# Kernel tuning notes

Hardware: AMD Instinct MI355X
Metric: run time of the kernel (lower is better)

Reference implementation:

```python
import jax, jax.numpy as jnp
import numpy as np

B, T, D, H, L, V = 2, 2048, 1024, 16, 12, 50257
HD = D // H          # head size 64
F = 4 * D            # FFN hidden 4096
EPS = 1e-5


def setup_inputs() -> dict:
    key = jax.random.key(0)
    keys = iter(jax.random.split(key, 16))
    n = lambda shape: jax.random.normal(next(keys), shape, jnp.float32) * 0.02
    inp = {
        "x": jax.random.randint(next(keys), (B, T), 0, V),
        "tok_emb": n((V, D)),
        "pos_emb": n((T, D)),
        "ln1_g": jnp.ones((L, D), jnp.float32), "ln1_b": jnp.zeros((L, D), jnp.float32),
        "wq": n((L, D, D)), "bq": jnp.zeros((L, D), jnp.float32),
        "wk": n((L, D, D)), "bk": jnp.zeros((L, D), jnp.float32),
        "wv": n((L, D, D)), "bv": jnp.zeros((L, D), jnp.float32),
        "wo": n((L, D, D)), "bo": jnp.zeros((L, D), jnp.float32),
        "ln2_g": jnp.ones((L, D), jnp.float32), "ln2_b": jnp.zeros((L, D), jnp.float32),
        "w1": n((L, D, F)), "b1": jnp.zeros((L, F), jnp.float32),
        "w2": n((L, F, D)), "b2": jnp.zeros((L, D), jnp.float32),
        "lnf_g": jnp.ones((D,), jnp.float32), "lnf_b": jnp.zeros((D,), jnp.float32),
        "fc_w": n((D, V)), "fc_b": jnp.zeros((V,), jnp.float32),
    }
    return inp


def _layernorm(x, g, b):
    m = jnp.mean(x, axis=-1, keepdims=True)
    v = jnp.var(x, axis=-1, keepdims=True)
    return (x - m) * jax.lax.rsqrt(v + EPS) * g + b


def _forward(x, tok_emb, pos_emb, ln1_g, ln1_b, wq, bq, wk, bk, wv, bv,
             wo, bo, ln2_g, ln2_b, w1, b1, w2, b2, lnf_g, lnf_b, fc_w, fc_b):
    # token + positional embedding (dropout is eval-mode identity)
    h = tok_emb[x] + pos_emb[None]                      # [B,T,D]
    mask = jnp.tril(jnp.ones((T, T), bool))             # causal mask
    scale = HD ** (-0.5)
    for l in range(L):
        # NOTE: original Block applies residual around the POST-norm activation
        hn = _layernorm(h, ln1_g[l], ln1_b[l])
        q = (hn @ wq[l] + bq[l]).reshape(B, T, H, HD)
        k = (hn @ wk[l] + bk[l]).reshape(B, T, H, HD)
        v = (hn @ wv[l] + bv[l]).reshape(B, T, H, HD)
        scores = jnp.einsum('bthd,bshd->bhts', q, k) * scale
        scores = jnp.where(mask[None, None], scores, -jnp.inf)
        attn = jax.nn.softmax(scores, axis=-1)
        o = jnp.einsum('bhts,bshd->bthd', attn, v).reshape(B, T, D)
        h = hn + (o @ wo[l] + bo[l])
        hn2 = _layernorm(h, ln2_g[l], ln2_b[l])
        h = hn2 + (jax.nn.relu(hn2 @ w1[l] + b1[l]) @ w2[l] + b2[l])
    h = _layernorm(h, lnf_g, lnf_b)
    logits = h @ fc_w + fc_b                            # [B,T,V]
    return logits


def reference(x, tok_emb, pos_emb, ln1_g, ln1_b, wq, bq, wk, bk, wv, bv,
              wo, bo, ln2_g, ln2_b, w1, b1, w2, b2, lnf_g, lnf_b, fc_w, fc_b):
    return _forward(x, tok_emb, pos_emb, ln1_g, ln1_b, wq, bq, wk, bk, wv, bv,
                    wo, bo, ln2_g, ln2_b, w1, b1, w2, b2, lnf_g, lnf_b, fc_w, fc_b)
```

## Files before the change

### kernel.cpp

```cpp
#include <hip/hip_runtime.h>

#define BB 2
#define TT 2048
#define DD 1024
#define HH 16
#define LL 12
#define VV 50257
#define VP 50432
#define HDD 64
#define FF 4096
#define MM (BB*TT)
#define QS 3072

typedef __bf16 bf16;
typedef __bf16 bf16x8 __attribute__((ext_vector_type(8)));
typedef __bf16 bf16x4 __attribute__((ext_vector_type(4)));
typedef __bf16 bf16x2 __attribute__((ext_vector_type(2)));
typedef float  f32x4  __attribute__((ext_vector_type(4)));
typedef float  f32x4u __attribute__((ext_vector_type(4), aligned(4)));
typedef unsigned int u32x4 __attribute__((ext_vector_type(4)));

typedef const __attribute__((address_space(1))) void* gas_t;
typedef __attribute__((address_space(3))) void* las_t;

__global__ __launch_bounds__(256) void k_embed(const int* __restrict__ x,
    const float* __restrict__ tok, const float* __restrict__ pos,
    float* __restrict__ h)
{
    int row = blockIdx.x;
    int t   = row & (TT - 1);
    int idx = x[row];
    int c   = threadIdx.x * 4;
    float4 a = *(const float4*)(tok + (size_t)idx * DD + c);
    float4 p = *(const float4*)(pos + (size_t)t   * DD + c);
    a.x += p.x; a.y += p.y; a.z += p.z; a.w += p.w;
    *(float4*)(h + (size_t)row * DD + c) = a;
}

__global__ __launch_bounds__(256) void k_ln(const float* __restrict__ in,
    const float* __restrict__ g, const float* __restrict__ b,
    float* __restrict__ outf, bf16* __restrict__ outb)
{
    int row = blockIdx.x, tid = threadIdx.x;
    const float4 v = *(const float4*)(in + (size_t)row * DD + tid * 4);
    float s  = v.x + v.y + v.z + v.w;
    float s2 = v.x*v.x + v.y*v.y + v.z*v.z + v.w*v.w;
    #pragma unroll
    for (int d = 1; d < 64; d <<= 1) { s += __shfl_xor(s, d); s2 += __shfl_xor(s2, d); }
    __shared__ float red[8];
    __shared__ float mv[2];
    int wid = tid >> 6, lane = tid & 63;
    if (lane == 0) { red[2*wid] = s; red[2*wid+1] = s2; }
    __syncthreads();
    if (tid == 0) {
        float ts  = red[0] + red[2] + red[4] + red[6];
        float ts2 = red[1] + red[3] + red[5] + red[7];
        float mean = ts * (1.0f / DD);
        float var  = ts2 * (1.0f / DD) - mean * mean;
        mv[0] = mean; mv[1] = 1.0f / sqrtf(var + 1e-5f);
    }
    __syncthreads();
    float mean = mv[0], inv = mv[1];
    float4 gg = *(const float4*)(g + tid * 4);
    float4 bb = *(const float4*)(b + tid * 4);
    float o0 = (v.x - mean) * inv * gg.x + bb.x;
    float o1 = (v.y - mean) * inv * gg.y + bb.y;
    float o2 = (v.z - mean) * inv * gg.z + bb.z;
    float o3 = (v.w - mean) * inv * gg.w + bb.w;
    size_t o = (size_t)row * DD + tid * 4;
    if (outf) { float4 r = {o0, o1, o2, o3}; *(float4*)(outf + o) = r; }
    if (outb) {
        bf16x4 r4 = {(bf16)o0, (bf16)o1, (bf16)o2, (bf16)o3};
        *(bf16x4*)(outb + o) = r4;
    }
}

__global__ __launch_bounds__(256) void k_wtrans(
    const float* __restrict__ src, bf16* __restrict__ dst,
    int K, int N, int Npad, size_t srcLS, size_t dstLS)
{
    src += (size_t)blockIdx.z * srcLS;
    dst += (size_t)blockIdx.z * dstLS;
    int k0 = blockIdx.y * 32, n0 = blockIdx.x * 256;
    __shared__ float tile[32][256];
    int tid = threadIdx.x;
    #pragma unroll
    for (int p = 0; p < 8; p++) {
        int kk = p * 4 + (tid >> 6);
        int nn = (tid & 63) * 4;
        const float* sp = src + (size_t)(k0 + kk) * N + n0 + nn;
        f32x4u v = {0.f, 0.f, 0.f, 0.f};
        if (n0 + nn + 3 < N) {
            v = *(const f32x4u*)sp;
        } else {
            #pragma unroll
            for (int i = 0; i < 4; i++)
                if (n0 + nn + i < N) v[i] = sp[i];
        }
        *(f32x4*)&tile[kk][nn] = v;
    }
    __syncthreads();
    int n = n0 + tid;
    if (n < Npad) {
        bf16 rowv[32];
        #pragma unroll
        for (int kk = 0; kk < 32; kk++) rowv[kk] = (bf16)tile[kk][tid];
        bf16* dp = dst + (size_t)n * K + k0;
        #pragma unroll
        for (int s = 0; s < 4; s++)
            *(bf16x8*)(dp + s * 8) = *(const bf16x8*)&rowv[s * 8];
    }
}

__global__ __launch_bounds__(256) void k_biasmerge(
    const float* __restrict__ bq, const float* __restrict__ bk,
    const float* __restrict__ bv, float* __restrict__ dst)
{
    int i = blockIdx.x * 256 + threadIdx.x;
    if (i >= LL * QS) return;
    int l = i / QS, j = i % QS;
    float v = (j < 1024) ? bq[l*1024 + j]
            : (j < 2048) ? bk[l*1024 + j - 1024]
                         : bv[l*1024 + j - 2048];
    dst[i] = v;
}

#define GEMM_EPILOGUE(MI_CNT, WM_STRIDE)                                        \
    bool nalign = ((Nout & 3) == 0);                                            \
    _Pragma("unroll")                                                           \
    for (int mi = 0; mi < MI_CNT; mi++) {                                       \
        int row = m0 + wm*WM_STRIDE + mi*16 + r16;                              \
        _Pragma("unroll")                                                       \
        for (int ni = 0; ni < 4; ni++) {                                        \
            int col0 = n0 + wn*64 + ni*16 + g4*4;                               \
            f32x4 v = acc[mi][ni];                                              \
            float sc = (qpre && col0 < 1024) ? 0.125f : 1.0f;                   \
            if (col0 + 3 < Nout) {                                              \
                if (bias) {                                                     \
                    float4 bi = *(const float4*)(bias + col0);                  \
                    v[0] += bi.x; v[1] += bi.y; v[2] += bi.z; v[3] += bi.w;     \
                }                                                               \
                if (res) {                                                      \
                    float4 rr = *(const float4*)(res + (size_t)row*Nout + col0);\
                    v[0] += rr.x; v[1] += rr.y; v[2] += rr.z; v[3] += rr.w;     \
                }                                                               \
                if (relu) { _Pragma("unroll")                                   \
                    for (int j = 0; j < 4; j++) v[j] = fmaxf(v[j], 0.0f); }     \
                if (outf) {                                                     \
                    float* p = outf + (size_t)row * Nout + col0;                \
                    if (nalign) *(f32x4*)p = v; else *(f32x4u*)p = v;           \
                }                                                               \
                if (outb) {                                                     \
                    bf16x4 o4 = {(bf16)(v[0]*sc), (bf16)(v[1]*sc),              \
                                 (bf16)(v[2]*sc), (bf16)(v[3]*sc)};             \
                    *(bf16x4*)(outb + (size_t)row * Nout + col0) = o4;          \
                }                                                               \
            } else {                                                            \
                _Pragma("unroll")                                               \
                for (int j = 0; j < 4; j++) {                                   \
                    int col = col0 + j;                                         \
                    if (col >= Nout) continue;                                  \
                    float vv = v[j] + (bias ? bias[col] : 0.0f);                \
                    if (res)  vv += res[(size_t)row * Nout + col];              \
                    if (relu) vv = fmaxf(vv, 0.0f);                             \
                    if (outf) outf[(size_t)row * Nout + col] = vv;              \
                    if (outb) outb[(size_t)row * Nout + col] = (bf16)(vv*sc);   \
                }                                                               \
            }                                                                   \
        }                                                                       \
    }

#define BARS { __builtin_amdgcn_sched_barrier(0); __builtin_amdgcn_s_barrier(); }

#define STG2(nn, kk)                                                            \
    do { const int k0_ = (nn)*64 + (kk)*32; const int db_ = (nn)&1;             \
        _Pragma("unroll") for (int i_ = 0; i_ < 2; i_++) {                      \
            int a_ = i_*2048 + tid*8;                                           \
            int sr_ = a_>>6, x_ = (a_&63) ^ ((sr_&7)<<3);                       \
            int r_ = 2*sr_ + (x_>>5), e_ = x_&31;                               \
            __builtin_amdgcn_global_load_lds(                                   \
                (gas_t)(A + (size_t)(m0+r_)*K + k0_+e_),                        \
                (las_t)&lA[db_][kk][a_], 16, 0, 0);                             \
        }                                                                       \
        _Pragma("unroll") for (int i_ = 0; i_ < 2; i_++) {                      \
            int a_ = i_*2048 + tid*8;                                           \
            int sr_ = a_>>6, x_ = (a_&63) ^ ((sr_&7)<<3);                       \
            int r_ = 2*sr_ + (x_>>5), e_ = x_&31;                               \
            __builtin_amdgcn_global_load_lds(                                   \
                (gas_t)(BT + (size_t)(n0+r_)*K + k0_+e_),                       \
                (las_t)&lB[db_][kk][a_], 16, 0, 0);                             \
        }                                                                       \
    } while (0)

#define PH2(nn, kk, sn, sk, wv)                                                 \
    { const int db_ = (nn)&1;                                                   \
        bf16x8 af[4], bfr[4];                                                   \
        _Pragma("unroll") for (int mi = 0; mi < 4; mi++) {                      \
            int row_ = wm*64 + mi*16 + r16;                                     \
            int sr_ = row_>>1;                                                  \
            int xp_ = (((row_&1)<<5) | kfrag) ^ ((sr_&7)<<3);                   \
            af[mi] = *(const bf16x8*)&lA[db_][kk][sr_*64 + xp_];                \
        }                                                                       \
        _Pragma("unroll") for (int ni = 0; ni < 4; ni++) {                      \
            int row_ = wn*64 + ni*16 + r16;                                     \
            int sr_ = row_>>1;                                                  \
            int xp_ = (((row_&1)<<5) | kfrag) ^ ((sr_&7)<<3);                   \
            bfr[ni] = *(const bf16x8*)&lB[db_][kk][sr_*64 + xp_];               \
        }                                                                       \
        bool st_ = (sn) < nt;                                                   \
        if (st_) STG2(sn, sk);                                                  \
        BARS;                                                                   \
        __builtin_amdgcn_s_setprio(1);                                          \
        _Pragma("unroll") for (int mi = 0; mi < 4; mi++)                        \
            _Pragma("unroll") for (int ni = 0; ni < 4; ni++)                    \
                acc[mi][ni] = __builtin_amdgcn_mfma_f32_16x16x32_bf16(          \
                    bfr[ni], af[mi], acc[mi][ni], 0, 0, 0);                     \
        __builtin_amdgcn_s_setprio(0);                                          \
        if (wv) { if (st_) asm volatile("s_waitcnt vmcnt(4)" ::: "memory");     \
                  else     asm volatile("s_waitcnt vmcnt(0)" ::: "memory"); }   \
        BARS;                                                                   \
    }

__global__ __launch_bounds__(256) void k_gemm2(
    const bf16* __restrict__ A, const bf16* __restrict__ BT,
    const float* __restrict__ bias, const float* __restrict__ res,
    float* __restrict__ outf, bf16* __restrict__ outb,
    int K, int Nout, int relu, int mswap, int qpre)
{
    __shared__ alignas(16) bf16 lA[2][2][128 * 32];
    __shared__ alignas(16) bf16 lB[2][2][128 * 32];
    int tid = threadIdx.x;
    int lane = tid & 63, w = tid >> 6;
    int wm = w >> 1, wn = w & 1;
    int nb = mswap ? blockIdx.y : blockIdx.x;
    int mb = mswap ? blockIdx.x : blockIdx.y;
    int n0 = nb * 128, m0 = mb * 128;
    int r16 = lane & 15, g4 = lane >> 4;
    int kfrag = g4 * 8;

    f32x4 acc[4][4];
    const f32x4 fzero = {0.f, 0.f, 0.f, 0.f};
    #pragma unroll
    for (int i = 0; i < 4; i++)
        #pragma unroll
        for (int j = 0; j < 4; j++) acc[i][j] = fzero;

    int nt = K >> 6;
    STG2(0, 0); STG2(0, 1); STG2(1, 0);
    asm volatile("s_waitcnt vmcnt(4)" ::: "memory");
    BARS;
    for (int it2 = 0; it2 < nt; it2 += 2) {
        PH2(it2,     0, it2 + 1, 1, 0);
        PH2(it2,     1, it2 + 2, 0, 1);
        PH2(it2 + 1, 0, it2 + 2, 1, 0);
        PH2(it2 + 1, 1, it2 + 3, 0, 1);
    }
    GEMM_EPILOGUE(4, 64)
}

#define SA3(tile, u)                                                            \
    do { int s_ = tid*8; int rl_ = s_>>6;                                       \
        int x_ = (s_&63) ^ ((rl_&7)<<3);                                        \
        __builtin_amdgcn_global_load_lds(                                       \
            (gas_t)(A + (size_t)(m0 + (u)*64 + rl_)*K + (size_t)(tile)*64 + x_),\
            (las_t)&lA3[(tile)&1][(u)*4096 + s_], 16, 0, 0);                    \
    } while (0)
#define SB3(tile, v)                                                            \
    do { int s_ = tid*8; int rl_ = s_>>6; int lr_ = (v)*64 + rl_;               \
        int r_ = (lr_ < 128) ? ((lr_&31) + ((lr_>>5)<<6))                       \
                             : (32 + ((lr_-128)&31) + (((lr_-128)>>5)<<6));     \
        int x_ = (s_&63) ^ ((rl_&7)<<3);                                        \
        __builtin_amdgcn_global_load_lds(                                       \
            (gas_t)(BT + (size_t)(n0 + r_)*K + (size_t)(tile)*64 + x_),         \
            (las_t)&lB3[(tile)&1][(v)*4096 + s_], 16, 0, 0);                    \
    } while (0)
#define RDA3(dst, mig, mi, kh) { int lr_ = wm*128 + ((mig)*4+(mi))*16 + r16;    \
    dst = *(const bf16x8*)&lA3[db_][lr_*64 + ((((kh)*32) | kfrag) ^ ((lr_&7)<<3))]; }
#define RDB3(dst, ni, kh) { int lr_ = wn*32 + (((ni)&1)<<4) + r16 + (((ni)>=2)?128:0); \
    dst = *(const bf16x8*)&lB3[db_][lr_*64 + ((((kh)*32) | kfrag) ^ ((lr_&7)<<3))]; }
#define MF3(mb_, nb_)                                                           \
    _Pragma("unroll") for (int kh = 0; kh < 2; kh++)                            \
        _Pragma("unroll") for (int mi = 0; mi < 4; mi++)                        \
            _Pragma("unroll") for (int ni = 0; ni < 2; ni++)                    \
                acc[(mb_)+mi][(nb_)+ni] = __builtin_amdgcn_mfma_f32_16x16x32_bf16( \
                    bfr[(nb_)+ni][kh], afr[mi][kh], acc[(mb_)+mi][(nb_)+ni], 0, 0, 0);

#define QUAD3(nn, cs, sn)                                                       \
    { const int db_ = (nn)&1;                                                   \
                                                                        \
      _Pragma("unroll") for (int mi=0;mi<4;mi++){RDA3(afr[mi][0],0,mi,0);RDA3(afr[mi][1],0,mi,1);} \
      _Pragma("unroll") for (int ni=0;ni<2;ni++){RDB3(bfr[ni][0],ni,0);RDB3(bfr[ni][1],ni,1);}     \
      BARS;                                                                     \
      __builtin_amdgcn_s_setprio(1); MF3(0,0); __builtin_amdgcn_s_setprio(0);   \
      BARS;                                                                     \
                                                                        \
      _Pragma("unroll") for (int ni=2;ni<4;ni++){RDB3(bfr[ni][0],ni,0);RDB3(bfr[ni][1],ni,1);}     \
      if (cs) { SA3(sn,0); SA3(sn,2); }                                         \
      BARS;                                                                     \
      __builtin_amdgcn_s_setprio(1); MF3(0,2); __builtin_amdgcn_s_setprio(0);   \
      BARS;                                                                     \
                                                                        \
      _Pragma("unroll") for (int mi=0;mi<4;mi++){RDA3(afr[mi][0],1,mi,0);RDA3(afr[mi][1],1,mi,1);} \
      if (cs) { SB3(sn,0); SB3(sn,1); SB3(sn,2); SB3(sn,3); }                   \
      BARS;                                                                     \
      __builtin_amdgcn_s_setprio(1); MF3(4,0); __builtin_amdgcn_s_setprio(0);   \
      BARS;                                                                     \
                                                                        \
      if (cs) { SA3(sn,1); SA3(sn,3); }                                         \
      BARS;                                                                     \
      __builtin_amdgcn_s_setprio(1); MF3(4,2); __builtin_amdgcn_s_setprio(0);   \
      if (cs) asm volatile("s_waitcnt vmcnt(8)" ::: "memory");                  \
      else    asm volatile("s_waitcnt vmcnt(0)" ::: "memory");                  \
      BARS; }

__global__ __launch_bounds__(512, 2) void k_gemm3(
    const bf16* __restrict__ A, const bf16* __restrict__ BT,
    const float* __restrict__ bias, const float* __restrict__ res,
    float* __restrict__ outf, bf16* __restrict__ outb,
    int K, int Nout, int relu, int mswap, int qpre)
{
    __shared__ alignas(16) bf16 lA3[2][256 * 64];
    __shared__ alignas(16) bf16 lB3[2][256 * 64];
    int tid = threadIdx.x;
    int lane = tid & 63, w = tid >> 6;
    int wm = w >> 2, wn = w & 3;
    int nb = mswap ? blockIdx.y : blockIdx.x;
    int mb = mswap ? blockIdx.x : blockIdx.y;
    int n0 = nb * 256, m0 = mb * 256;
    int r16 = lane & 15, g4 = lane >> 4;
    int kfrag = g4 * 8;

    f32x4 acc[8][4];
    const f32x4 fzero = {0.f, 0.f, 0.f, 0.f};
    #pragma unroll
    for (int i = 0; i < 8; i++)
        #pragma unroll
        for (int j = 0; j < 4; j++) acc[i][j] = fzero;

    bf16x8 afr[4][2];
    bf16x8 bfr[4][2];

    int nt = K >> 6;
    SA3(0,0); SA3(0,1); SA3(0,2); SA3(0,3);
    SB3(0,0); SB3(0,1); SB3(0,2); SB3(0,3);
    SA3(1,0); SA3(1,1); SA3(1,2); SA3(1,3);
    SB3(1,0); SB3(1,1); SB3(1,2); SB3(1,3);
    asm volatile("s_waitcnt vmcnt(8)" ::: "memory");
    BARS;
    for (int it2 = 0; it2 < nt; it2 += 2) {
        bool c2 = (it2 + 2 < nt), c3 = (it2 + 3 < nt);
        QUAD3(it2,     c2, it2 + 2);
        QUAD3(it2 + 1, c3, it2 + 3);
    }
    GEMM_EPILOGUE(8, 128)
}

__global__ __launch_bounds__(256) void k_gemm_f32b(
    const bf16* __restrict__ A, const float* __restrict__ Bm,
    const float* __restrict__ bias, float* __restrict__ outf,
    int M, int N, int K)
{
    __shared__ alignas(16) bf16 lA[128][40];
    __shared__ alignas(16) bf16 lB[128][40];
    int tid  = threadIdx.x;
    int lane = tid & 63, wid = tid >> 6;
    int wm = wid >> 1, wn = wid & 1;
    int m0 = blockIdx.x * 128, n0 = blockIdx.y * 128;
    int r16 = lane & 15, g4 = lane >> 4;

    f32x4 acc[4][4];
    const f32x4 fzero = {0.f, 0.f, 0.f, 0.f};
    #pragma unroll
    for (int i = 0; i < 4; i++)
        #pragma unroll
        for (int j = 0; j < 4; j++) acc[i][j] = fzero;

    int arow = tid >> 2, aseg = tid & 3;
    int bkr  = tid >> 3, bnb  = tid & 7;
    bool nfull = (n0 + 128 <= N);

    for (int k0 = 0; k0 < K; k0 += 32) {
        *(uint4*)&lA[arow][aseg*8] =
            *(const uint4*)(A + (size_t)(m0 + arow) * K + k0 + aseg*8);
        *(uint4*)&lA[arow + 64][aseg*8] =
            *(const uint4*)(A + (size_t)(m0 + arow + 64) * K + k0 + aseg*8);
        const float* bsrc = Bm + (size_t)(k0 + bkr) * N + n0;
        #pragma unroll
        for (int q = 0; q < 4; q++) {
            int n = q*32 + bnb*4;
            #pragma unroll
            for (int i = 0; i < 4; i++) {
                float fv = 0.0f;
                if (nfull || (n0 + n + i < N)) fv = bsrc[n + i];
                lB[n+i][bkr] = (bf16)fv;
            }
        }
        __syncthreads();
        int kb = g4 * 8;
        bf16x8 af[4], bfr[4];
        #pragma unroll
        for (int mi = 0; mi < 4; mi++)
            af[mi] = *(const bf16x8*)&lA[wm*64 + mi*16 + r16][kb];
        #pragma unroll
        for (int ni = 0; ni < 4; ni++)
            bfr[ni] = *(const bf16x8*)&lB[wn*64 + ni*16 + r16][kb];
        #pragma unroll
        for (int mi = 0; mi < 4; mi++)
            #pragma unroll
            for (int ni = 0; ni < 4; ni++)
                acc[mi][ni] = __builtin_amdgcn_mfma_f32_16x16x32_bf16(
                    af[mi], bfr[ni], acc[mi][ni], 0, 0, 0);
        __syncthreads();
    }

    #pragma unroll
    for (int ni = 0; ni < 4; ni++) {
        int col = n0 + wn*64 + ni*16 + r16;
        if (col >= N) continue;
        float bi = bias[col];
        #pragma unroll
        for (int mi = 0; mi < 4; mi++) {
            #pragma unroll
            for (int j = 0; j < 4; j++) {
                int row = m0 + wm*64 + mi*16 + g4*4 + j;
                outf[(size_t)row * N + col] = acc[mi][ni][j] + bi;
            }
        }
    }
}

__global__ __launch_bounds__(512) void k_attn3(
    const bf16* __restrict__ qkv, bf16* __restrict__ o)
{
    __shared__ alignas(16) bf16 lK[64][72];
    __shared__ alignas(16) bf16 lVT[64][72];
    int tid = threadIdx.x, lane = tid & 63, w = tid >> 6;
    int r16 = lane & 15, g4 = lane >> 4;
    int t0 = blockIdx.x * 128;
    int bh = blockIdx.y, bb = bh >> 4, hh = bh & 15;
    const bf16* base = qkv + (size_t)bb * TT * QS + hh * HDD;
    const bf16* kp = base + 1024;
    const bf16* vp = base + 2048;
    bf16* op = o + (size_t)bb * TT * DD + hh * HDD;
    int qrow = t0 + w * 16;

    bf16x8 qf0, qf1;
    {
        const bf16* qr = base + (size_t)(qrow + r16) * QS + g4 * 8;
        qf0 = *(const bf16x8*)qr;
        qf1 = *(const bf16x8*)(qr + 32);
    }

    int krow = tid >> 3, kseg = tid & 7;
    int vsp  = tid >> 4, vseg = tid & 15;

    f32x4 oacc[4];
    const f32x4 fzero = {0.f, 0.f, 0.f, 0.f};
    #pragma unroll
    for (int i = 0; i < 4; i++) oacc[i] = fzero;
    float mrun = -1e30f, lrun = 0.f;

    int send = t0 + 128;
    bf16x8 kr;
    bf16x4 va4, vb4;
    {
        kr  = *(const bf16x8*)(kp + (size_t)krow * QS + kseg * 8);
        va4 = *(const bf16x4*)(vp + (size_t)(2*vsp) * QS + vseg * 4);
        vb4 = *(const bf16x4*)(vp + (size_t)(2*vsp) * QS + QS + vseg * 4);
    }

    for (int s0 = 0; s0 < send; s0 += 64) {
        __syncthreads();
        *(bf16x8*)&lK[krow][kseg*8] = kr;
        #pragma unroll
        for (int i = 0; i < 4; i++) {
            int d = vseg*4 + i;
            int mpr = (vsp >> 2) ^ (d >> 3);
            bf16x2 pv2 = {va4[i], vb4[i]};
            *(unsigned int*)&lVT[d][mpr*8 + (vsp&3)*2] =
                __builtin_bit_cast(unsigned int, pv2);
        }
        if (s0 + 64 < send) {
            kr  = *(const bf16x8*)(kp + (size_t)(s0 + 64 + krow) * QS + kseg * 8);
            va4 = *(const bf16x4*)(vp + (size_t)(s0 + 64 + 2*vsp) * QS + vseg * 4);
            vb4 = *(const bf16x4*)(vp + (size_t)(s0 + 64 + 2*vsp) * QS + QS + vseg * 4);
        }
        __syncthreads();

        if (s0 <= qrow + 15) {
            f32x4 sf[4];
            __builtin_amdgcn_s_setprio(1);
            #pragma unroll
            for (int nf = 0; nf < 4; nf++) {
                sf[nf] = fzero;
                bf16x8 kf0 = *(const bf16x8*)&lK[nf*16 + r16][g4*8];
                bf16x8 kf1 = *(const bf16x8*)&lK[nf*16 + r16][32 + g4*8];
                sf[nf] = __builtin_amdgcn_mfma_f32_16x16x32_bf16(kf0, qf0, sf[nf], 0, 0, 0);
                sf[nf] = __builtin_amdgcn_mfma_f32_16x16x32_bf16(kf1, qf1, sf[nf], 0, 0, 0);
            }
            __builtin_amdgcn_s_setprio(0);
            int qa = qrow + r16;
            if (s0 + 63 > qrow) {
                #pragma unroll
                for (int nf = 0; nf < 4; nf++)
                    #pragma unroll
                    for (int j = 0; j < 4; j++)
                        if (s0 + nf*16 + g4*4 + j > qa) sf[nf][j] = -1e30f;
            }
            float pm = sf[0][0];
            #pragma unroll
            for (int nf = 0; nf < 4; nf++)
                #pragma unroll
                for (int j = 0; j < 4; j++) pm = fmaxf(pm, sf[nf][j]);
            pm = fmaxf(pm, __shfl_xor(pm, 16));
            pm = fmaxf(pm, __shfl_xor(pm, 32));
            bool defer = (__all(pm - mrun <= 8.0f) != 0);
            float al = 1.0f;
            if (!defer) {
                float mn = fmaxf(mrun, pm);
                al = __expf(mrun - mn);
                mrun = mn;
            }
            float ps = 0.f;
            #pragma unroll
            for (int nf = 0; nf < 4; nf++)
                #pragma unroll
                for (int j = 0; j < 4; j++) {
                    float p = __expf(sf[nf][j] - mrun);
                    sf[nf][j] = p;
                    ps += p;
                }
            ps += __shfl_xor(ps, 16);
            ps += __shfl_xor(ps, 32);
            lrun = lrun * al + ps;
            if (!defer) {
                #pragma unroll
                for (int nf = 0; nf < 4; nf++)
                    #pragma unroll
                    for (int j = 0; j < 4; j++) oacc[nf][j] *= al;
            }
            unsigned int pk[4][2];
            #pragma unroll
            for (int nf = 0; nf < 4; nf++) {
                bf16x2 a = {(bf16)sf[nf][0], (bf16)sf[nf][1]};
                bf16x2 b = {(bf16)sf[nf][2], (bf16)sf[nf][3]};
                pk[nf][0] = __builtin_bit_cast(unsigned int, a);
                pk[nf][1] = __builtin_bit_cast(unsigned int, b);
            }
            int srcA = r16 + (2*(g4 & 1))*16;
            int srcB = srcA + 16;
            bool hi2 = (g4 >= 2);
            __builtin_amdgcn_s_setprio(1);
            #pragma unroll
            for (int c = 0; c < 2; c++) {
                unsigned int a0 = __shfl(pk[2*c  ][0], srcA);
                unsigned int a1 = __shfl(pk[2*c+1][0], srcA);
                unsigned int b0 = __shfl(pk[2*c  ][1], srcA);
                unsigned int b1 = __shfl(pk[2*c+1][1], srcA);
                unsigned int e0 = __shfl(pk[2*c  ][0], srcB);
                unsigned int e1 = __shfl(pk[2*c+1][0], srcB);
                unsigned int f0 = __shfl(pk[2*c  ][1], srcB);
                unsigned int f1 = __shfl(pk[2*c+1][1], srcB);
                u32x4 uu = { hi2 ? a1 : a0, hi2 ? b1 : b0,
                             hi2 ? e1 : e0, hi2 ? f1 : f0 };
                bf16x8 pf = __builtin_bit_cast(bf16x8, uu);
                #pragma unroll
                for (int nf = 0; nf < 4; nf++) {
                    int d = nf*16 + r16;
                    int mread = (4*c + g4) ^ (d >> 3);
                    bf16x8 vt = *(const bf16x8*)&lVT[d][mread*8];
                    oacc[nf] = __builtin_amdgcn_mfma_f32_16x16x32_bf16(
                        vt, pf, oacc[nf], 0, 0, 0);
                }
            }
            __builtin_amdgcn_s_setprio(0);
        }
    }

    float inv = 1.0f / lrun;
    #pragma unroll
    for (int nf = 0; nf < 4; nf++) {
        f32x4 ov = oacc[nf];
        bf16x4 o4 = {(bf16)(ov[0]*inv), (bf16)(ov[1]*inv),
                     (bf16)(ov[2]*inv), (bf16)(ov[3]*inv)};
        *(bf16x4*)(op + (size_t)(qrow + r16) * DD + nf*16 + g4*4) = o4;
    }
}

extern "C" void kernel_launch(void* const* d_in, const int* in_sizes, int n_in,
                              void* d_out, int out_size, void* d_ws, size_t ws_size,
                              hipStream_t stream)
{
    (void)in_sizes; (void)n_in; (void)out_size;
    const int*   x    = (const int*)  d_in[0];
    const float* tok  = (const float*)d_in[1];
    const float* pos  = (const float*)d_in[2];
    const float* ln1g = (const float*)d_in[3];
    const float* ln1b = (const float*)d_in[4];
    const float* wq   = (const float*)d_in[5];
    const float* bq   = (const float*)d_in[6];
    const float* wk   = (const float*)d_in[7];
    const float* bk   = (const float*)d_in[8];
    const float* wv   = (const float*)d_in[9];
    const float* bv   = (const float*)d_in[10];
    const float* wo   = (const float*)d_in[11];
    const float* bo   = (const float*)d_in[12];
    const float* ln2g = (const float*)d_in[13];
    const float* ln2b = (const float*)d_in[14];
    const float* w1   = (const float*)d_in[15];
    const float* b1   = (const float*)d_in[16];
    const float* w2   = (const float*)d_in[17];
    const float* b2   = (const float*)d_in[18];
    const float* lnfg = (const float*)d_in[19];
    const float* lnfb = (const float*)d_in[20];
    const float* fcw  = (const float*)d_in[21];
    const float* fcb  = (const float*)d_in[22];

    const size_t MB = (size_t)1 << 20;
    char*  sb   = (char*)d_out;
    float* h    = (float*)(sb);
    float* hn   = (float*)(sb + 16*MB);
    bf16*  hnb  = (bf16*) (sb + 32*MB);
    bf16*  qkv  = (bf16*) (sb + 40*MB);
    bf16*  obuf = (bf16*) (sb + 64*MB);
    bf16*  f1b  = (bf16*) (sb + 72*MB);
    bf16*  WT   = (bf16*) (sb + 104*MB);
    float* bqkv = (float*)(sb + 392*MB);
    bf16*  hfb  = (bf16*) d_ws;

    const size_t LWT = 12582912;
    const size_t FCWT_BYTES = (size_t)VP * DD * 2;
    bool fast_logits = (ws_size >= 8*MB + FCWT_BYTES);
    bf16* fcwT = (bf16*)((char*)d_ws + 8*MB);

    dim3 blk(256);
    dim3 blk512(512);

    k_wtrans<<<dim3(4, 32, 12), blk, 0, stream>>>(wq, WT,               DD, DD, DD, (size_t)DD*DD, LWT);
    k_wtrans<<<dim3(4, 32, 12), blk, 0, stream>>>(wk, WT + 1024*1024,   DD, DD, DD, (size_t)DD*DD, LWT);
    k_wtrans<<<dim3(4, 32, 12), blk, 0, stream>>>(wv, WT + 2048*1024,   DD, DD, DD, (size_t)DD*DD, LWT);
    k_wtrans<<<dim3(4, 32, 12), blk, 0, stream>>>(wo, WT + 3145728,     DD, DD, DD, (size_t)DD*DD, LWT);
    k_wtrans<<<dim3(16, 32, 12), blk, 0, stream>>>(w1, WT + 4194304,    DD, FF, FF, (size_t)DD*FF, LWT);
    k_wtrans<<<dim3(4, 128, 12), blk, 0, stream>>>(w2, WT + 8388608,    FF, DD, DD, (size_t)FF*DD, LWT);
    if (fast_logits)
        k_wtrans<<<dim3(VP/256, 32, 1), blk, 0, stream>>>(fcw, fcwT, DD, VV, VP, 0, 0);
    k_biasmerge<<<dim3(144), blk, 0, stream>>>(bq, bk, bv, bqkv);

    k_embed<<<MM, blk, 0, stream>>>(x, tok, pos, h);
    for (int l = 0; l < LL; l++) {
        const bf16* WTl = WT + (size_t)l * LWT;
        k_ln<<<MM, blk, 0, stream>>>(h, ln1g + l*DD, ln1b + l*DD, hn, hnb);
        k_gemm2<<<dim3(24, 32), blk, 0, stream>>>(hnb, WTl, bqkv + l*QS,
                                                  nullptr, nullptr, qkv, DD, QS, 0, 0, 1);
        k_attn3<<<dim3(TT/128, BB*HH), blk512, 0, stream>>>(qkv, obuf);
        k_gemm2<<<dim3(8, 32), blk, 0, stream>>>(obuf, WTl + 3145728, bo + l*DD,
                                                 hn, h, nullptr, DD, DD, 0, 0, 0);
        k_ln<<<MM, blk, 0, stream>>>(h, ln2g + l*DD, ln2b + l*DD, hn, hnb);
        k_gemm3<<<dim3(FF/256, MM/256), blk512, 0, stream>>>(hnb, WTl + 4194304, b1 + l*FF,
                                                  nullptr, nullptr, f1b, DD, FF, 1, 0, 0);
        k_gemm2<<<dim3(8, 32), blk, 0, stream>>>(f1b, WTl + 8388608, b2 + l*DD,
                                                 hn, h, nullptr, FF, DD, 0, 0, 0);
    }
    k_ln<<<MM, blk, 0, stream>>>(h, lnfg, lnfb, nullptr, hfb);

    if (fast_logits) {
        k_gemm3<<<dim3(MM/256, VP/256), blk512, 0, stream>>>(hfb, fcwT, fcb,
                                                      nullptr, (float*)d_out, nullptr,
                                                      DD, VV, 0, 1, 0);
    } else {
        k_gemm_f32b<<<dim3(32, (VV + 127)/128), blk, 0, stream>>>(hfb, fcw, fcb,
                                                                  (float*)d_out, MM, VV, DD);
    }
}
```

Before: 4.498 ms.

## Template gemm2 on M-tile, use 64-row tiles for N=1024 GEMMs, nontemporal logits stores

```diff
diff --git a/kernel.cpp b/kernel.cpp
--- a/kernel.cpp
+++ b/kernel.cpp
@@ -148,7 +148,11 @@
                     for (int j = 0; j < 4; j++) v[j] = fmaxf(v[j], 0.0f); }     \
                 if (outf) {                                                     \
                     float* p = outf + (size_t)row * Nout + col0;                \
-                    if (nalign) *(f32x4*)p = v; else *(f32x4u*)p = v;           \
+                    if (ntflag) {                                               \
+                        f32x4u vv = v;                                          \
+                        __builtin_nontemporal_store(vv, (f32x4u*)p);            \
+                    } else if (nalign) *(f32x4*)p = v;                          \
+                    else *(f32x4u*)p = v;                                       \
                 }                                                               \
                 if (outb) {                                                     \
                     bf16x4 o4 = {(bf16)(v[0]*sc), (bf16)(v[1]*sc),              \
@@ -174,7 +178,7 @@
 
 #define STG2(nn, kk)                                                            \
     do { const int k0_ = (nn)*64 + (kk)*32; const int db_ = (nn)&1;             \
-        _Pragma("unroll") for (int i_ = 0; i_ < 2; i_++) {                      \
+        _Pragma("unroll") for (int i_ = 0; i_ < AL; i_++) {                     \
             int a_ = i_*2048 + tid*8;                                           \
             int sr_ = a_>>6, x_ = (a_&63) ^ ((sr_&7)<<3);                       \
             int r_ = 2*sr_ + (x_>>5), e_ = x_&31;                               \
@@ -192,11 +196,15 @@
         }                                                                       \
     } while (0)
 
+#define WAITG                                                                   \
+    { if constexpr (MT == 128) asm volatile("s_waitcnt vmcnt(4)" ::: "memory"); \
+      else                     asm volatile("s_waitcnt vmcnt(3)" ::: "memory"); }
+
 #define PH2(nn, kk, sn, sk, wv)                                                 \
     { const int db_ = (nn)&1;                                                   \
-        bf16x8 af[4], bfr[4];                                                   \
-        _Pragma("unroll") for (int mi = 0; mi < 4; mi++) {                      \
-            int row_ = wm*64 + mi*16 + r16;                                     \
+        bf16x8 af[MI], bfr[4];                                                  \
+        _Pragma("unroll") for (int mi = 0; mi < MI; mi++) {                     \
+            int row_ = wm*(MT/2) + mi*16 + r16;                                 \
             int sr_ = row_>>1;                                                  \
             int xp_ = (((row_&1)<<5) | kfrag) ^ ((sr_&7)<<3);                   \
             af[mi] = *(const bf16x8*)&lA[db_][kk][sr_*64 + xp_];                \
@@ -211,43 +219,47 @@
         if (st_) STG2(sn, sk);                                                  \
         BARS;                                                                   \
         __builtin_amdgcn_s_setprio(1);                                          \
-        _Pragma("unroll") for (int mi = 0; mi < 4; mi++)                        \
+        _Pragma("unroll") for (int mi = 0; mi < MI; mi++)                       \
             _Pragma("unroll") for (int ni = 0; ni < 4; ni++)                    \
                 acc[mi][ni] = __builtin_amdgcn_mfma_f32_16x16x32_bf16(          \
                     bfr[ni], af[mi], acc[mi][ni], 0, 0, 0);                     \
         __builtin_amdgcn_s_setprio(0);                                          \
-        if (wv) { if (st_) asm volatile("s_waitcnt vmcnt(4)" ::: "memory");     \
+        if (wv) { if (st_) WAITG                                                \
                   else     asm volatile("s_waitcnt vmcnt(0)" ::: "memory"); }   \
         BARS;                                                                   \
     }
 
-__global__ __launch_bounds__(256) void k_gemm2(
+template<int MT>
+__global__ __launch_bounds__(256) void k_gemm2t(
     const bf16* __restrict__ A, const bf16* __restrict__ BT,
     const float* __restrict__ bias, const float* __restrict__ res,
     float* __restrict__ outf, bf16* __restrict__ outb,
     int K, int Nout, int relu, int mswap, int qpre)
 {
-    __shared__ alignas(16) bf16 lA[2][2][128 * 32];
+    constexpr int AL = MT / 64;
+    constexpr int MI = MT / 32;
+    __shared__ alignas(16) bf16 lA[2][2][MT * 32];
     __shared__ alignas(16) bf16 lB[2][2][128 * 32];
     int tid = threadIdx.x;
     int lane = tid & 63, w = tid >> 6;
     int wm = w >> 1, wn = w & 1;
     int nb = mswap ? blockIdx.y : blockIdx.x;
     int mb = mswap ? blockIdx.x : blockIdx.y;
-    int n0 = nb * 128, m0 = mb * 128;
+    int n0 = nb * 128, m0 = mb * MT;
     int r16 = lane & 15, g4 = lane >> 4;
     int kfrag = g4 * 8;
-
-    f32x4 acc[4][4];
+    const int ntflag = 0;
+
+    f32x4 acc[MI][4];
     const f32x4 fzero = {0.f, 0.f, 0.f, 0.f};
     #pragma unroll
-    for (int i = 0; i < 4; i++)
+    for (int i = 0; i < MI; i++)
         #pragma unroll
         for (int j = 0; j < 4; j++) acc[i][j] = fzero;
 
     int nt = K >> 6;
     STG2(0, 0); STG2(0, 1); STG2(1, 0);
-    asm volatile("s_waitcnt vmcnt(4)" ::: "memory");
+    WAITG
     BARS;
     for (int it2 = 0; it2 < nt; it2 += 2) {
         PH2(it2,     0, it2 + 1, 1, 0);
@@ -255,7 +267,7 @@
         PH2(it2 + 1, 0, it2 + 2, 1, 0);
         PH2(it2 + 1, 1, it2 + 3, 0, 1);
     }
-    GEMM_EPILOGUE(4, 64)
+    GEMM_EPILOGUE(MI, (MT/2))
 }
 
 #define SA3(tile, u)                                                            \
@@ -317,7 +329,7 @@
     const bf16* __restrict__ A, const bf16* __restrict__ BT,
     const float* __restrict__ bias, const float* __restrict__ res,
     float* __restrict__ outf, bf16* __restrict__ outb,
-    int K, int Nout, int relu, int mswap, int qpre)
+    int K, int Nout, int relu, int mswap, int qpre, int ntout)
 {
     __shared__ alignas(16) bf16 lA3[2][256 * 64];
     __shared__ alignas(16) bf16 lB3[2][256 * 64];
@@ -329,6 +341,7 @@
     int n0 = nb * 256, m0 = mb * 256;
     int r16 = lane & 15, g4 = lane >> 4;
     int kfrag = g4 * 8;
+    const int ntflag = ntout;
 
     f32x4 acc[8][4];
     const f32x4 fzero = {0.f, 0.f, 0.f, 0.f};
@@ -650,15 +663,15 @@
     for (int l = 0; l < LL; l++) {
         const bf16* WTl = WT + (size_t)l * LWT;
         k_ln<<<MM, blk, 0, stream>>>(h, ln1g + l*DD, ln1b + l*DD, hn, hnb);
-        k_gemm2<<<dim3(24, 32), blk, 0, stream>>>(hnb, WTl, bqkv + l*QS,
+        k_gemm2t<128><<<dim3(24, 32), blk, 0, stream>>>(hnb, WTl, bqkv + l*QS,
                                                   nullptr, nullptr, qkv, DD, QS, 0, 0, 1);
         k_attn3<<<dim3(TT/128, BB*HH), blk512, 0, stream>>>(qkv, obuf);
-        k_gemm2<<<dim3(8, 32), blk, 0, stream>>>(obuf, WTl + 3145728, bo + l*DD,
+        k_gemm2t<64><<<dim3(8, 64), blk, 0, stream>>>(obuf, WTl + 3145728, bo + l*DD,
                                                  hn, h, nullptr, DD, DD, 0, 0, 0);
         k_ln<<<MM, blk, 0, stream>>>(h, ln2g + l*DD, ln2b + l*DD, hn, hnb);
-        k_gemm3<<<dim3(FF/256, MM/256), blk512, 0, stream>>>(hnb, WTl + 4194304, b1 + l*FF,
+        k_gemm2t<128><<<dim3(32, 32), blk, 0, stream>>>(hnb, WTl + 4194304, b1 + l*FF,
                                                   nullptr, nullptr, f1b, DD, FF, 1, 0, 0);
-        k_gemm2<<<dim3(8, 32), blk, 0, stream>>>(f1b, WTl + 8388608, b2 + l*DD,
+        k_gemm2t<64><<<dim3(8, 64), blk, 0, stream>>>(f1b, WTl + 8388608, b2 + l*DD,
                                                  hn, h, nullptr, FF, DD, 0, 0, 0);
     }
     k_ln<<<MM, blk, 0, stream>>>(h, lnfg, lnfb, nullptr, hfb);
@@ -666,7 +679,7 @@
     if (fast_logits) {
         k_gemm3<<<dim3(MM/256, VP/256), blk512, 0, stream>>>(hfb, fcwT, fcb,
                                                       nullptr, (float*)d_out, nullptr,
-                                                      DD, VV, 0, 1, 0);
+                                                      DD, VV, 0, 1, 0, 1);
     } else {
         k_gemm_f32b<<<dim3(32, (VV + 127)/128), blk, 0, stream>>>(hfb, fcw, fcb,
                                                                   (float*)d_out, MM, VV, DD);
```

After: 4.785 ms. +6.4%, slower.
